# Kernel tuning notes

Hardware: AMD Instinct MI355X
Metric: run time of the kernel (lower is better)

Reference implementation:

```python
import jax, jax.numpy as jnp
import numpy as np

N_BLOCKS, B0, B1 = 128, 8, 8
OUT = N_BLOCKS * B0   # 1024
IN = N_BLOCKS * B1    # 1024 (cond_dim = None)
BATCH = 16384


def _masks():
    # block_diag_mask / block_tril_mask from flowjax (structural int32 constants)
    diag = np.zeros((OUT, IN), np.int32)
    tril = np.zeros((OUT, IN), np.int32)
    for i in range(N_BLOCKS):
        diag[i * B0:(i + 1) * B0, i * B1:(i + 1) * B1] = 1
        tril[(i + 1) * B0:, i * B1:(i + 1) * B1] = 1
    return jnp.asarray(diag), jnp.asarray(tril)


def setup_inputs() -> dict:
    key = jax.random.key(0)
    kx, kw, kb, ks = jax.random.split(key, 4)
    b_diag_mask, b_tril_mask = _masks()
    limit = float(np.sqrt(6.0 / (OUT + IN)))  # glorot_uniform
    W = jax.random.uniform(kw, (OUT, IN), jnp.float32, -limit, limit) * (b_diag_mask + b_tril_mask)
    bias = (jax.random.uniform(kb, (OUT,), jnp.float32) - 0.5) * (2.0 / np.sqrt(OUT))
    W_log_scale = jnp.log(jax.random.uniform(ks, (OUT, 1), jnp.float32, 1e-3, 1.0))
    x = jax.random.normal(kx, (BATCH, IN), jnp.float32)
    return {"x": x, "W": W, "bias": bias, "W_log_scale": W_log_scale,
            "b_diag_mask": b_diag_mask, "b_tril_mask": b_tril_mask}


def reference(x, W, bias, W_log_scale, b_diag_mask, b_tril_mask):
    # weight normalisation: exp() on diag blocks, identity on strictly-lower blocks,
    # per-row L2 norm, then learned scale
    Wm = jnp.exp(W) * b_diag_mask + W * b_tril_mask            # [OUT, IN]
    W_norms = jnp.linalg.norm(Wm, axis=-1, keepdims=True)      # [OUT, 1]
    Wn = jnp.exp(W_log_scale) * Wm / W_norms                   # [OUT, IN]
    # batched block-triangular matvec (vmap of W @ x + bias over batch)
    y = x @ Wn.T + bias                                        # [BATCH, OUT]
    # gather diagonal blocks -> (n_blocks, B0, B1), same row-major order as
    # jnp.where(b_diag_mask) indexing in the original
    idx = jnp.arange(N_BLOCKS)
    jac_3d = Wn.reshape(N_BLOCKS, B0, N_BLOCKS, B1)[idx, :, idx, :]  # [N_BLOCKS, B0, B1]
    return y, jnp.log(jac_3d)
```

## Files before the change

### kernel.cpp

```cpp
#include <hip/hip_runtime.h>

#define IN_DIM   1024
#define OUT_DIM  1024
#define BATCH    16384

#define BM 128
#define BN 256
#define BK 32

typedef __attribute__((ext_vector_type(8))) short          bf16x8;
typedef __attribute__((ext_vector_type(8))) unsigned short u16x8;
typedef __attribute__((ext_vector_type(4))) unsigned short u16x4;
typedef __attribute__((ext_vector_type(4))) float          f32x4;

__device__ __forceinline__ unsigned short f2bf(float f) {
    unsigned u = __float_as_uint(f);
    u += 0x7FFFu + ((u >> 16) & 1u);
    return (unsigned short)(u >> 16);
}
__device__ __forceinline__ float bf2f(unsigned short h) {
    return __uint_as_float((unsigned)h << 16);
}

#define GLOAD_LDS16(g, l)                                                      \
    __builtin_amdgcn_global_load_lds(                                          \
        (const __attribute__((address_space(1))) unsigned int*)(g),            \
        (__attribute__((address_space(3))) unsigned int*)(l), 16, 0, 0)

#define LGKM_BARRIER()                                                         \
    do {                                                                       \
        asm volatile("s_waitcnt lgkmcnt(0)" ::: "memory");                     \
        __builtin_amdgcn_sched_barrier(0);                                     \
        __builtin_amdgcn_s_barrier();                                          \
        __builtin_amdgcn_sched_barrier(0);                                     \
    } while (0)

__global__ __launch_bounds__(256) void prep_kernel(
    const float* __restrict__ W, const float* __restrict__ wls,
    unsigned short* __restrict__ wh, unsigned short* __restrict__ wl,
    float* __restrict__ jac)
{
    const int warp = threadIdx.x >> 6;
    const int lane = threadIdx.x & 63;
    const int row  = blockIdx.x * 4 + warp;
    const int r    = row >> 3;
    const int d0   = r * 8;
    const int nk   = d0 + 8;
    const float* Wr = W + (size_t)row * IN_DIM;

    float ss = 0.f;
    for (int k = lane * 4; k < nk; k += 256) {
        float4 v = *(const float4*)&Wr[k];
        if (k >= d0) { v.x = expf(v.x); v.y = expf(v.y); v.z = expf(v.z); v.w = expf(v.w); }
        ss += v.x * v.x + v.y * v.y + v.z * v.z + v.w * v.w;
    }
    #pragma unroll
    for (int off = 32; off >= 1; off >>= 1) ss += __shfl_xor(ss, off);

    const float lscale = wls[row] - 0.5f * logf(ss);
    const float scale  = expf(lscale);

    for (int k = lane * 4; k < IN_DIM; k += 256) {
        float4 v = {0.f, 0.f, 0.f, 0.f};
        if (k < nk) {
            v = *(const float4*)&Wr[k];
            if (k >= d0) { v.x = expf(v.x); v.y = expf(v.y); v.z = expf(v.z); v.w = expf(v.w); }
            v.x *= scale; v.y *= scale; v.z *= scale; v.w *= scale;
        }
        u16x4 h, l;
        const float f[4] = {v.x, v.y, v.z, v.w};
        #pragma unroll
        for (int i = 0; i < 4; ++i) {
            h[i] = f2bf(f[i]);
            l[i] = f2bf(f[i] - bf2f(h[i]));
        }
        *(u16x4*)&wh[(size_t)row * IN_DIM + k] = h;
        *(u16x4*)&wl[(size_t)row * IN_DIM + k] = l;
    }
    if (lane < 8) jac[r * 64 + (row & 7) * 8 + lane] = lscale + Wr[d0 + lane];
}

__global__ __launch_bounds__(512, 2) void gemm_kernel(
    const float* __restrict__ x,
    const unsigned short* __restrict__ wh, const unsigned short* __restrict__ wl,
    const float* __restrict__ bias, float* __restrict__ y)
{
    __shared__ __align__(16) unsigned short smem[65536];

    const int bid = (int)blockIdx.x;
    const int seg = bid >> 7;
    const int sb  = bid & 127;
    const int nt  = 3 - seg;
    const int mt  = (sb & 7) * 16 + (sb >> 3);
    const int m0  = mt * BM;
    const int n0  = nt * BN;
    const int nsteps = (n0 + BN) >> 5;

    const int t    = threadIdx.x;
    const int lane = t & 63;
    const int wid  = t >> 6;
    const int wr   = wid >> 2;
    const int wc   = wid & 3;
    const int lr   = lane & 15;
    const int lq   = lane >> 4;

    const float* xg = x + (size_t)(m0 + wid * 16 + lr) * IN_DIM + lq * 8;

    const size_t wsrc = (size_t)(n0 + wid * 32 + lr) * IN_DIM + lq * 8;
    const unsigned short* whg = wh + wsrc;
    const unsigned short* wlg = wl + wsrc;

    unsigned short* const xs  = smem;
    unsigned short* const wsm = smem + 16384;

    f32x4 acc[4][4];
    #pragma unroll
    for (int i = 0; i < 4; ++i)
        #pragma unroll
        for (int j = 0; j < 4; ++j) acc[i][j] = (f32x4){0.f, 0.f, 0.f, 0.f};

    float4 xva, xvb;

    auto LOAD_X = [&](int k0) {
        xva = *(const float4*)(xg + k0);
        xvb = *(const float4*)(xg + k0 + 4);
    };
    auto STAGE_W = [&](int b, int k0) {
        unsigned short* dh = wsm + b * 16384 + wid * 1024;
        unsigned short* dl = dh + 8192;
        GLOAD_LDS16(whg + k0,                dh);
        GLOAD_LDS16(whg + k0 + 16 * IN_DIM,  dh + 512);
        GLOAD_LDS16(wlg + k0,                dl);
        GLOAD_LDS16(wlg + k0 + 16 * IN_DIM,  dl + 512);
    };
    auto CVT_X = [&](int b) {
        unsigned short* dh = xs + b * 8192;
        const float f[8] = {xva.x, xva.y, xva.z, xva.w, xvb.x, xvb.y, xvb.z, xvb.w};
        u16x8 h, l;
        #pragma unroll
        for (int i = 0; i < 8; ++i) {
            h[i] = f2bf(f[i]);
            l[i] = f2bf(f[i] - bf2f(h[i]));
        }
        *(u16x8*)&dh[t * 8]        = h;
        *(u16x8*)&dh[4096 + t * 8] = l;
    };
    auto COMPUTE = [&](int xb, int wbuf) {
        const unsigned short* xh_ = xs + xb * 8192;
        const unsigned short* xl_ = xh_ + 4096;
        const unsigned short* wh_ = wsm + wbuf * 16384;
        const unsigned short* wl_ = wh_ + 8192;
        const int ao = wr * 2048 + lane * 8;
        const int bo = wc * 2048 + lane * 8;
        bf16x8 bh[4], bl[4];
        #pragma unroll
        for (int fc = 0; fc < 4; ++fc) {
            bh[fc] = *(const bf16x8*)&wh_[bo + fc * 512];
            bl[fc] = *(const bf16x8*)&wl_[bo + fc * 512];
        }
        #pragma unroll
        for (int fr = 0; fr < 4; ++fr) {
            const bf16x8 ah = *(const bf16x8*)&xh_[ao + fr * 512];
            const bf16x8 al = *(const bf16x8*)&xl_[ao + fr * 512];
            #pragma unroll
            for (int fc = 0; fc < 4; ++fc) {
                acc[fr][fc] = __builtin_amdgcn_mfma_f32_16x16x32_bf16(ah, bh[fc], acc[fr][fc], 0, 0, 0);
                acc[fr][fc] = __builtin_amdgcn_mfma_f32_16x16x32_bf16(ah, bl[fc], acc[fr][fc], 0, 0, 0);
                acc[fr][fc] = __builtin_amdgcn_mfma_f32_16x16x32_bf16(al, bh[fc], acc[fr][fc], 0, 0, 0);
            }
        }
    };

    STAGE_W(0, 0);
    LOAD_X(0);
    STAGE_W(1, BK);
    CVT_X(0);
    LGKM_BARRIER();

    int xb = 0, wb = 0, wb2 = 2;
    int k0 = 0;
    for (int i = 0; i < nsteps; ++i, k0 += BK) {
        const bool has1 = (i + 1) < nsteps;
        const bool has2 = (i + 2) < nsteps;
        if (has1) LOAD_X(k0 + BK);
        if (has2) {
            STAGE_W(wb2, k0 + 2 * BK);
            wb2 = (wb2 == 2) ? 0 : wb2 + 1;
        }
        COMPUTE(xb, wb);
        wb = (wb == 2) ? 0 : wb + 1;
        if (has1) {
            CVT_X(xb ^ 1);
            LGKM_BARRIER();
            xb ^= 1;
        }
    }
    __syncthreads();

    float* yt = (float*)smem;
    const int erow = t >> 2;
    const int ec0  = (t & 3) * 4;
    #pragma unroll
    for (int h = 0; h < 2; ++h) {
        if ((wc >> 1) == h) {
            #pragma unroll
            for (int fr = 0; fr < 4; ++fr) {
                const int row0 = wr * 64 + fr * 16 + lq * 4;
                #pragma unroll
                for (int fc = 0; fc < 4; ++fc) {
                    const int col = (wc & 1) * 64 + fc * 16 + lr;
                    #pragma unroll
                    for (int i = 0; i < 4; ++i)
                        yt[(row0 + i) * 132 + col] = acc[fr][fc][i];
                }
            }
        }
        __syncthreads();
        #pragma unroll
        for (int j = 0; j < 8; ++j) {
            const int col = ec0 + j * 16;
            float4 v = *(const float4*)&yt[erow * 132 + col];
            const float4 bb = *(const float4*)&bias[n0 + h * 128 + col];
            v.x += bb.x; v.y += bb.y; v.z += bb.z; v.w += bb.w;
            *(float4*)&y[(size_t)(m0 + erow) * OUT_DIM + n0 + h * 128 + col] = v;
        }
        __syncthreads();
    }
}

extern "C" void kernel_launch(void* const* d_in, const int* in_sizes, int n_in,
                              void* d_out, int out_size, void* d_ws, size_t ws_size,
                              hipStream_t stream)
{
    const float* x    = (const float*)d_in[0];
    const float* W    = (const float*)d_in[1];
    const float* bias = (const float*)d_in[2];
    const float* wls  = (const float*)d_in[3];

    unsigned short* wh = (unsigned short*)d_ws;
    unsigned short* wl = wh + (size_t)OUT_DIM * IN_DIM;
    float* y   = (float*)d_out;
    float* jac = y + (size_t)BATCH * OUT_DIM;

    prep_kernel<<<OUT_DIM / 4, 256, 0, stream>>>(W, wls, wh, wl, jac);

    gemm_kernel<<<4 * 128, 512, 0, stream>>>(x, wh, wl, bias, y);
}
```

Baseline: 201.4 us.

## Shrink GEMM tile to 128x128 with 256 threads and simple double buffering

The N tile width is halved to 128 and the block drops to 4 waves of 256 threads, with twice as many blocks in the grid. The three-stage W ring and split X buffers become a single double-buffered smem region, and each iteration now ends in a plain __syncthreads. Each thread loads and converts two rows of x. Smaller tiles give finer-grained triangular load balance and lower LDS use, which may allow more resident blocks. In exchange, x is reloaded more often relative to the work done and the pipelining depth is reduced.

```diff
diff --git a/kernel.cpp b/kernel.cpp
--- a/kernel.cpp
+++ b/kernel.cpp
@@ -5,7 +5,7 @@
 #define BATCH    16384
 
 #define BM 128
-#define BN 256
+#define BN 128
 #define BK 32
 
 typedef __attribute__((ext_vector_type(8))) short          bf16x8;
@@ -26,14 +26,6 @@
     __builtin_amdgcn_global_load_lds(                                          \
         (const __attribute__((address_space(1))) unsigned int*)(g),            \
         (__attribute__((address_space(3))) unsigned int*)(l), 16, 0, 0)
-
-#define LGKM_BARRIER()                                                         \
-    do {                                                                       \
-        asm volatile("s_waitcnt lgkmcnt(0)" ::: "memory");                     \
-        __builtin_amdgcn_sched_barrier(0);                                     \
-        __builtin_amdgcn_s_barrier();                                          \
-        __builtin_amdgcn_sched_barrier(0);                                     \
-    } while (0)
 
 __global__ __launch_bounds__(256) void prep_kernel(
     const float* __restrict__ W, const float* __restrict__ wls,
@@ -80,17 +72,17 @@
     if (lane < 8) jac[r * 64 + (row & 7) * 8 + lane] = lscale + Wr[d0 + lane];
 }
 
-__global__ __launch_bounds__(512, 2) void gemm_kernel(
+__global__ __launch_bounds__(256, 2) void gemm_kernel(
     const float* __restrict__ x,
     const unsigned short* __restrict__ wh, const unsigned short* __restrict__ wl,
     const float* __restrict__ bias, float* __restrict__ y)
 {
-    __shared__ __align__(16) unsigned short smem[65536];
+    __shared__ __align__(16) unsigned short smem[32768];
 
     const int bid = (int)blockIdx.x;
     const int seg = bid >> 7;
     const int sb  = bid & 127;
-    const int nt  = 3 - seg;
+    const int nt  = 7 - seg;
     const int mt  = (sb & 7) * 16 + (sb >> 3);
     const int m0  = mt * BM;
     const int n0  = nt * BN;
@@ -99,19 +91,17 @@
     const int t    = threadIdx.x;
     const int lane = t & 63;
     const int wid  = t >> 6;
-    const int wr   = wid >> 2;
-    const int wc   = wid & 3;
+    const int wr   = wid >> 1;
+    const int wc   = wid & 1;
     const int lr   = lane & 15;
     const int lq   = lane >> 4;
 
-    const float* xg = x + (size_t)(m0 + wid * 16 + lr) * IN_DIM + lq * 8;
-
-    const size_t wsrc = (size_t)(n0 + wid * 32 + lr) * IN_DIM + lq * 8;
-    const unsigned short* whg = wh + wsrc;
-    const unsigned short* wlg = wl + wsrc;
-
-    unsigned short* const xs  = smem;
-    unsigned short* const wsm = smem + 16384;
+    const int mA = ((t >> 6) & 3) * 16 + (t & 15);
+    const int kA = ((t >> 4) & 3) * 8;
+    const float* xg = x + (size_t)(m0 + mA) * IN_DIM + kA;
+
+    const unsigned short* whg = wh + (size_t)(n0 + wid * 32 + lr) * IN_DIM + lq * 8;
+    const unsigned short* wlg = wl + (size_t)(n0 + wid * 32 + lr) * IN_DIM + lq * 8;
 
     f32x4 acc[4][4];
     #pragma unroll
@@ -119,37 +109,43 @@
         #pragma unroll
         for (int j = 0; j < 4; ++j) acc[i][j] = (f32x4){0.f, 0.f, 0.f, 0.f};
 
-    float4 xva, xvb;
+    float4 xva, xvb, xvc, xvd;
 
     auto LOAD_X = [&](int k0) {
         xva = *(const float4*)(xg + k0);
         xvb = *(const float4*)(xg + k0 + 4);
+        xvc = *(const float4*)(xg + 64 * IN_DIM + k0);
+        xvd = *(const float4*)(xg + 64 * IN_DIM + k0 + 4);
     };
     auto STAGE_W = [&](int b, int k0) {
-        unsigned short* dh = wsm + b * 16384 + wid * 1024;
-        unsigned short* dl = dh + 8192;
-        GLOAD_LDS16(whg + k0,                dh);
-        GLOAD_LDS16(whg + k0 + 16 * IN_DIM,  dh + 512);
-        GLOAD_LDS16(wlg + k0,                dl);
-        GLOAD_LDS16(wlg + k0 + 16 * IN_DIM,  dl + 512);
+        unsigned short* whp = smem + b * 16384 + 8192  + wid * 1024;
+        unsigned short* wlp = smem + b * 16384 + 12288 + wid * 1024;
+        GLOAD_LDS16(whg + k0,                whp);
+        GLOAD_LDS16(whg + k0 + 16 * IN_DIM,  whp + 512);
+        GLOAD_LDS16(wlg + k0,                wlp);
+        GLOAD_LDS16(wlg + k0 + 16 * IN_DIM,  wlp + 512);
     };
     auto CVT_X = [&](int b) {
-        unsigned short* dh = xs + b * 8192;
-        const float f[8] = {xva.x, xva.y, xva.z, xva.w, xvb.x, xvb.y, xvb.z, xvb.w};
-        u16x8 h, l;
+        unsigned short* xhp = smem + b * 16384;
+        unsigned short* xlp = xhp + 4096;
+        const float fa[8] = {xva.x, xva.y, xva.z, xva.w, xvb.x, xvb.y, xvb.z, xvb.w};
+        const float fb[8] = {xvc.x, xvc.y, xvc.z, xvc.w, xvd.x, xvd.y, xvd.z, xvd.w};
+        u16x8 h0, l0, h1, l1;
         #pragma unroll
         for (int i = 0; i < 8; ++i) {
-            h[i] = f2bf(f[i]);
-            l[i] = f2bf(f[i] - bf2f(h[i]));
-        }
-        *(u16x8*)&dh[t * 8]        = h;
-        *(u16x8*)&dh[4096 + t * 8] = l;
-    };
-    auto COMPUTE = [&](int xb, int wbuf) {
-        const unsigned short* xh_ = xs + xb * 8192;
+            h0[i] = f2bf(fa[i]);  l0[i] = f2bf(fa[i] - bf2f(h0[i]));
+            h1[i] = f2bf(fb[i]);  l1[i] = f2bf(fb[i] - bf2f(h1[i]));
+        }
+        *(u16x8*)&xhp[t * 8]        = h0;
+        *(u16x8*)&xlp[t * 8]        = l0;
+        *(u16x8*)&xhp[2048 + t * 8] = h1;
+        *(u16x8*)&xlp[2048 + t * 8] = l1;
+    };
+    auto COMPUTE = [&](int b) {
+        const unsigned short* xh_ = smem + b * 16384;
         const unsigned short* xl_ = xh_ + 4096;
-        const unsigned short* wh_ = wsm + wbuf * 16384;
-        const unsigned short* wl_ = wh_ + 8192;
+        const unsigned short* wh_ = xh_ + 8192;
+        const unsigned short* wl_ = xh_ + 12288;
         const int ao = wr * 2048 + lane * 8;
         const int bo = wc * 2048 + lane * 8;
         bf16x8 bh[4], bl[4];
@@ -171,44 +167,37 @@
         }
     };
 
+    LOAD_X(0);
     STAGE_W(0, 0);
-    LOAD_X(0);
-    STAGE_W(1, BK);
     CVT_X(0);
-    LGKM_BARRIER();
-
-    int xb = 0, wb = 0, wb2 = 2;
+    __syncthreads();
+
+    int buf = 0;
     int k0 = 0;
     for (int i = 0; i < nsteps; ++i, k0 += BK) {
         const bool has1 = (i + 1) < nsteps;
-        const bool has2 = (i + 2) < nsteps;
-        if (has1) LOAD_X(k0 + BK);
-        if (has2) {
-            STAGE_W(wb2, k0 + 2 * BK);
-            wb2 = (wb2 == 2) ? 0 : wb2 + 1;
-        }
-        COMPUTE(xb, wb);
-        wb = (wb == 2) ? 0 : wb + 1;
         if (has1) {
-            CVT_X(xb ^ 1);
-            LGKM_BARRIER();
-            xb ^= 1;
-        }
-    }
-    __syncthreads();
+            LOAD_X(k0 + BK);
+            STAGE_W(buf ^ 1, k0 + BK);
+        }
+        COMPUTE(buf);
+        if (has1) CVT_X(buf ^ 1);
+        __syncthreads();
+        buf ^= 1;
+    }
 
     float* yt = (float*)smem;
-    const int erow = t >> 2;
-    const int ec0  = (t & 3) * 4;
+    const int er = t >> 2;
+    const int ec = (t & 3) * 4;
     #pragma unroll
     for (int h = 0; h < 2; ++h) {
-        if ((wc >> 1) == h) {
+        if (wr == h) {
             #pragma unroll
             for (int fr = 0; fr < 4; ++fr) {
-                const int row0 = wr * 64 + fr * 16 + lq * 4;
+                const int row0 = fr * 16 + lq * 4;
                 #pragma unroll
                 for (int fc = 0; fc < 4; ++fc) {
-                    const int col = (wc & 1) * 64 + fc * 16 + lr;
+                    const int col = wc * 64 + fc * 16 + lr;
                     #pragma unroll
                     for (int i = 0; i < 4; ++i)
                         yt[(row0 + i) * 132 + col] = acc[fr][fc][i];
@@ -218,11 +207,11 @@
         __syncthreads();
         #pragma unroll
         for (int j = 0; j < 8; ++j) {
-            const int col = ec0 + j * 16;
-            float4 v = *(const float4*)&yt[erow * 132 + col];
-            const float4 bb = *(const float4*)&bias[n0 + h * 128 + col];
+            const int col = ec + j * 16;
+            float4 v = *(const float4*)&yt[er * 132 + col];
+            const float4 bb = *(const float4*)&bias[n0 + col];
             v.x += bb.x; v.y += bb.y; v.z += bb.z; v.w += bb.w;
-            *(float4*)&y[(size_t)(m0 + erow) * OUT_DIM + n0 + h * 128 + col] = v;
+            *(float4*)&y[(size_t)(m0 + h * 64 + er) * OUT_DIM + n0 + col] = v;
         }
         __syncthreads();
     }
@@ -244,5 +233,5 @@
 
     prep_kernel<<<OUT_DIM / 4, 256, 0, stream>>>(W, wls, wh, wl, jac);
 
-    gemm_kernel<<<4 * 128, 512, 0, stream>>>(x, wh, wl, bias, y);
-}
+    gemm_kernel<<<8 * 128, 256, 0, stream>>>(x, wh, wl, bias, y);
+}
```

Result: faster. 191.9 us (-4.7%).
